# Performance work log

Measured on AMD Instinct MI355X. Metric: run time of the kernel, lower is better.

Reference implementation:

```python
import jax, jax.numpy as jnp
import numpy as np

EMBED_DIM = 1024
NUM_HEADS = 16
HEAD_DIM = EMBED_DIM // NUM_HEADS
T, B = 2048, 2


def setup_inputs() -> dict:
    key = jax.random.key(0)
    ks = jax.random.split(key, 12)
    s = 1.0 / np.sqrt(EMBED_DIM)
    x = jax.random.normal(ks[0], (T, B, EMBED_DIM), dtype=jnp.float32)
    time_decay = jax.random.uniform(ks[1], (T, B, 1), dtype=jnp.float32)
    # causal mask: masked_fill where mask == 0
    attn_mask = jnp.tril(jnp.ones((T, T), dtype=jnp.int32))
    Wq = jax.random.uniform(ks[2], (EMBED_DIM, EMBED_DIM), jnp.float32, -s, s)
    bq = jax.random.uniform(ks[3], (EMBED_DIM,), jnp.float32, -s, s)
    Wk = jax.random.uniform(ks[4], (EMBED_DIM, EMBED_DIM), jnp.float32, -s, s)
    bk = jax.random.uniform(ks[5], (EMBED_DIM,), jnp.float32, -s, s)
    Wv = jax.random.uniform(ks[6], (EMBED_DIM, EMBED_DIM), jnp.float32, -s, s)
    bv = jax.random.uniform(ks[7], (EMBED_DIM,), jnp.float32, -s, s)
    Wo = jax.random.uniform(ks[8], (EMBED_DIM, EMBED_DIM), jnp.float32, -s, s)
    bo = jax.random.uniform(ks[9], (EMBED_DIM,), jnp.float32, -s, s)
    return {"x": x, "time_decay": time_decay, "attn_mask": attn_mask,
            "Wq": Wq, "bq": bq, "Wk": Wk, "bk": bk,
            "Wv": Wv, "bv": bv, "Wo": Wo, "bo": bo}


def reference(x, time_decay, attn_mask, Wq, bq, Wk, bk, Wv, bv, Wo, bo):
    t, b, e = x.shape
    h, d = NUM_HEADS, HEAD_DIM
    # linear (torch: y = x @ W.T + b), then split heads -> (B, H, T, D)
    def proj(W, bias):
        y = jnp.einsum('tbe,fe->tbf', x, W) + bias
        return y.reshape(t, b, h, d).transpose(1, 2, 0, 3)
    Q, K, V = proj(Wq, bq), proj(Wk, bk), proj(Wv, bv)
    scores = jnp.einsum('bhqd,bhkd->bhqk', Q, K) / np.sqrt(d).astype(jnp.float32)
    scores = jnp.where(attn_mask == 0, jnp.float32(-1e9), scores)
    attn = jax.nn.softmax(scores, axis=-1)
    out = jnp.einsum('bhqk,bhkd->bhqd', attn, V)      # (B,H,T,D)
    out = out.transpose(2, 0, 1, 3).reshape(t, b, e)   # (T,B,E)
    out = jnp.einsum('tbe,fe->tbf', out, Wo) + bo
    return out * time_decay
```

## Files before the change

### kernel.cpp

```cpp
#include <hip/hip_runtime.h>


typedef unsigned short u16;
typedef unsigned int u32;
typedef __attribute__((ext_vector_type(8))) short bf16x8_t;
typedef __attribute__((ext_vector_type(4))) float fx4_t;

#define T_SEQ 2048
#define BATCH 2
#define EMB   1024
#define NH    16
#define HD    64
#define MROWS (T_SEQ * BATCH)

#define EXP2F(x) __builtin_amdgcn_exp2f(x)

__device__ __forceinline__ float bf2f(u16 u) {
  union { unsigned int i; float f; } v;
  v.i = ((unsigned int)u) << 16;
  return v.f;
}
__device__ __forceinline__ u16 f2bf(float f) {
  union { float f; unsigned int i; } v;
  v.f = f;
  unsigned int x = v.i;
  unsigned int r = (x + 0x7fffu + ((x >> 16) & 1u)) >> 16;
  return (u16)r;
}
__device__ __forceinline__ u32 fbits(float f) {
  union { float f; u32 i; } v; v.f = f; return v.i;
}

__device__ __forceinline__ void glds16(const void* g, void* l) {
  __builtin_amdgcn_global_load_lds(
      (const __attribute__((address_space(1))) unsigned int*)g,
      (__attribute__((address_space(3))) unsigned int*)l, 16, 0, 0);
}


__global__ void cvt_all(const float* __restrict__ x,
                        const float* __restrict__ wq, const float* __restrict__ wk,
                        const float* __restrict__ wv, const float* __restrict__ wo,
                        u16* __restrict__ xb,
                        u16* __restrict__ wqb, u16* __restrict__ wkb,
                        u16* __restrict__ wvb, u16* __restrict__ wob) {
  int i = blockIdx.x * blockDim.x + threadIdx.x;
  const float* src; u16* dst; int off;
  if (i < 1048576)      { src = x;  dst = xb;  off = i; }
  else if (i < 1310720) { src = wq; dst = wqb; off = i - 1048576; }
  else if (i < 1572864) { src = wk; dst = wkb; off = i - 1310720; }
  else if (i < 1835008) { src = wv; dst = wvb; off = i - 1572864; }
  else                  { src = wo; dst = wob; off = i - 1835008; }
  float4 v = ((const float4*)src)[off];
  ushort4 o;
  o.x = f2bf(v.x); o.y = f2bf(v.y); o.z = f2bf(v.z); o.w = f2bf(v.w);
  ((ushort4*)dst)[off] = o;
}

__global__ __launch_bounds__(256, 3) void gemm_qkv(
    const u16* __restrict__ xb,
    const u16* __restrict__ wq, const u16* __restrict__ wk, const u16* __restrict__ wv,
    const float* __restrict__ bq, const float* __restrict__ bk, const float* __restrict__ bv,
    u16* __restrict__ Qm, u16* __restrict__ Km, u16* __restrict__ VTg) {
  __shared__ short As[2][128 * 64];
  __shared__ short Bs[2][64 * 64];

  const int z = blockIdx.z;
  const u16* W = (z == 0) ? wq : (z == 1) ? wk : wv;
  const float* bias = (z == 0) ? bq : (z == 1) ? bk : bv;

  const int tid = threadIdx.x;
  const int bm = blockIdx.x, bn = blockIdx.y;
  const int lane = tid & 63, w = tid >> 6;
  const int wm = w >> 1, wn = w & 1;
  const int lr = lane & 15, quad = lane >> 4;
  const int r0 = lane >> 3;
  const int c8s = ((lane & 7) ^ r0) * 8;
  const int sw = (lr & 7);

  fx4_t acc[4][2];
#pragma unroll
  for (int i = 0; i < 4; i++)
#pragma unroll
    for (int j = 0; j < 2; j++) acc[i][j] = (fx4_t){0.f, 0.f, 0.f, 0.f};

#define STAGE(kt_, bi_)                                                          \
  {                                                                              \
    const int k0_ = (kt_) * 64;                                                  \
    _Pragma("unroll")                                                            \
    for (int i = 0; i < 4; i++) {             \
      const int rr = w * 32 + i * 8;                                             \
      const int ml = bm * 128 + rr + r0;                                         \
      const int grow = (z == 2) ? (((ml & 2047) << 1) | (ml >> 11)) : ml;        \
      glds16(xb + (size_t)grow * EMB + k0_ + c8s, &As[bi_][rr * 64]);            \
    }                                                                            \
    _Pragma("unroll")                                                            \
    for (int i = 0; i < 2; i++) {              \
      const int rr = w * 16 + i * 8;                                             \
      glds16(W + (size_t)(bn * 64 + rr + r0) * EMB + k0_ + c8s,                  \
             &Bs[bi_][rr * 64]);                                                 \
    }                                                                            \
  }

  const int nkt = EMB / 64;
  STAGE(0, 0);
  __syncthreads();

  for (int kt = 0; kt < nkt; kt++) {
    const int buf = kt & 1;
    if (kt + 1 < nkt) STAGE(kt + 1, buf ^ 1);
#pragma unroll
    for (int ks = 0; ks < 2; ++ks) {
      bf16x8_t a[4], b[2];
#pragma unroll
      for (int i = 0; i < 4; i++)
        a[i] = *(const bf16x8_t*)&As[buf][(wm * 64 + i * 16 + lr) * 64 + (((ks * 4 + quad) ^ sw) * 8)];
#pragma unroll
      for (int j = 0; j < 2; j++)
        b[j] = *(const bf16x8_t*)&Bs[buf][(wn * 32 + j * 16 + lr) * 64 + (((ks * 4 + quad) ^ sw) * 8)];
      if (z == 2) {
#pragma unroll
        for (int i = 0; i < 4; i++)
#pragma unroll
          for (int j = 0; j < 2; j++)
            acc[i][j] = __builtin_amdgcn_mfma_f32_16x16x32_bf16(b[j], a[i], acc[i][j], 0, 0, 0);
      } else {
#pragma unroll
        for (int i = 0; i < 4; i++)
#pragma unroll
          for (int j = 0; j < 2; j++)
            acc[i][j] = __builtin_amdgcn_mfma_f32_16x16x32_bf16(a[i], b[j], acc[i][j], 0, 0, 0);
      }
    }
    __syncthreads();
  }
#undef STAGE

  if (z == 2) {
#pragma unroll
    for (int i = 0; i < 4; i++) {
#pragma unroll
      for (int j = 0; j < 2; j++) {
#pragma unroll
        for (int r = 0; r < 4; r++) {
          const int n = bn * 64 + wn * 32 + j * 16 + quad * 4 + r;
          const int ml = bm * 128 + wm * 64 + i * 16 + lr;
          const int t = ml & 2047, bb = ml >> 11;
          const int h = n >> 6, d = n & 63;
          VTg[((size_t)(bb * NH + h) * HD + d) * T_SEQ + t] = f2bf(acc[i][j][r] + bias[n]);
        }
      }
    }
  } else {
    u16* dst = (z == 0) ? Qm : Km;
#pragma unroll
    for (int i = 0; i < 4; i++) {
#pragma unroll
      for (int j = 0; j < 2; j++) {
        const int n = bn * 64 + wn * 32 + j * 16 + lr;
        const float bsv = bias[n];
#pragma unroll
        for (int r = 0; r < 4; r++) {
          const int m = bm * 128 + wm * 64 + i * 16 + quad * 4 + r;
          dst[(size_t)m * EMB + n] = f2bf(acc[i][j][r] + bsv);
        }
      }
    }
  }
}

__global__ __launch_bounds__(256, 2) void gemm_out(
    const u16* __restrict__ Ob, const u16* __restrict__ wo,
    const float* __restrict__ bo, const float* __restrict__ td,
    float* __restrict__ out) {
  __shared__ short As[64 * 64];
  __shared__ short Bs[128 * 64];

  const int tid = threadIdx.x;
  const int bm = blockIdx.x, bn = blockIdx.y;
  const int lane = tid & 63, w = tid >> 6;
  const int wm = w >> 1, wn = w & 1;
  const int lr = lane & 15, quad = lane >> 4;
  const int r0 = lane >> 3;
  const int c8s = ((lane & 7) ^ r0) * 8;
  const int sw = (lr & 7);

  fx4_t acc[2][4];
#pragma unroll
  for (int i = 0; i < 2; i++)
#pragma unroll
    for (int j = 0; j < 4; j++) acc[i][j] = (fx4_t){0.f, 0.f, 0.f, 0.f};

  for (int k0 = 0; k0 < EMB; k0 += 64) {
#pragma unroll
    for (int i = 0; i < 2; i++) {
      const int rr = w * 16 + i * 8;
      glds16(Ob + (size_t)(bm * 64 + rr + r0) * EMB + k0 + c8s, &As[rr * 64]);
    }
#pragma unroll
    for (int i = 0; i < 4; i++) {
      const int rr = w * 32 + i * 8;
      glds16(wo + (size_t)(bn * 128 + rr + r0) * EMB + k0 + c8s, &Bs[rr * 64]);
    }
    __syncthreads();
#pragma unroll
    for (int ks = 0; ks < 2; ++ks) {
      bf16x8_t a[2], b[4];
#pragma unroll
      for (int i = 0; i < 2; i++)
        a[i] = *(const bf16x8_t*)&As[(wm * 32 + i * 16 + lr) * 64 + (((ks * 4 + quad) ^ sw) * 8)];
#pragma unroll
      for (int j = 0; j < 4; j++)
        b[j] = *(const bf16x8_t*)&Bs[(wn * 64 + j * 16 + lr) * 64 + (((ks * 4 + quad) ^ sw) * 8)];
#pragma unroll
      for (int i = 0; i < 2; i++)
#pragma unroll
        for (int j = 0; j < 4; j++)
          acc[i][j] = __builtin_amdgcn_mfma_f32_16x16x32_bf16(a[i], b[j], acc[i][j], 0, 0, 0);
    }
    __syncthreads();
  }

#pragma unroll
  for (int i = 0; i < 2; i++) {
#pragma unroll
    for (int j = 0; j < 4; j++) {
      const int n = bn * 128 + wn * 64 + j * 16 + lr;
      const float bsv = bo[n];
#pragma unroll
      for (int r = 0; r < 4; r++) {
        const int m = bm * 64 + wm * 32 + i * 16 + quad * 4 + r;
        out[(size_t)m * EMB + n] = (acc[i][j][r] + bsv) * td[m];
      }
    }
  }
}

__global__ __launch_bounds__(256, 2) void attn_bal(
    const u16* __restrict__ Qm, const u16* __restrict__ Km, const u16* __restrict__ VTg,
    u16* __restrict__ Ob) {
  __shared__ short Kd[3][64 * 64];
  __shared__ short Vd[3][64 * 64];
  __shared__ short Ps[4][16 * 72];

  const int blk = blockIdx.x;
  const int bh = blk & 31;
  const int p = blk >> 5;
  const int b = bh >> 4, h = bh & 15;

  const int tid = threadIdx.x;
  const int w = tid >> 6, lane = tid & 63;
  const int lr = lane & 15, quad = lane >> 4;
  const int r0 = lane >> 3;
  const int c8s = ((lane & 7) ^ r0) * 8;
  const int sw = (lr & 7);

  const u16* Qbase = Qm + (size_t)b * EMB + (size_t)h * HD;
  const u16* Kbase = Km + (size_t)b * EMB + (size_t)h * HD;
  const u16* VTb = VTg + (size_t)bh * HD * T_SEQ;

  const float QSCALE = 0.18033688f;

#define STAGE(kt_, buf_)                                                            \
  {                                                                                 \
    const int k0_ = (kt_) * 64;                                                     \
    _Pragma("unroll")                                                               \
    for (int i = 0; i < 2; i++) {                                                   \
      const int rr = w * 16 + i * 8;                                                \
      glds16(Kbase + (size_t)(k0_ + rr + r0) * 2 * EMB + c8s, &Kd[buf_][rr * 64]);  \
      glds16(VTb + (size_t)(rr + r0) * T_SEQ + k0_ + c8s, &Vd[buf_][rr * 64]);      \
    }                                                                               \
  }
#define WAIT4()  asm volatile("s_waitcnt vmcnt(4)" ::: "memory")
#define WAIT0()  asm volatile("s_waitcnt vmcnt(0)" ::: "memory")
#define BAR()    asm volatile("s_barrier" ::: "memory")

  for (int job = 0; job < 2; ++job) {
    const int qt = job ? (31 - p) : p;
    const int qb = qt * 64;

    bf16x8_t qf[2];
#pragma unroll
    for (int ks = 0; ks < 2; ks++) {
      bf16x8_t v = *(const bf16x8_t*)(Qbase + (size_t)(qb + w * 16 + lr) * 2 * EMB + ks * 32 + quad * 8);
      bf16x8_t o;
#pragma unroll
      for (int e = 0; e < 8; e++) o[e] = (short)f2bf(bf2f((u16)v[e]) * QSCALE);
      qf[ks] = o;
    }

    fx4_t acc_o[4];
#pragma unroll
    for (int dn = 0; dn < 4; dn++) acc_o[dn] = (fx4_t){0.f, 0.f, 0.f, 0.f};
    float l_par = 0.f;

    const int nkt = qt + 1;
    STAGE(0, 0);
    if (nkt > 1) { STAGE(1, 1); WAIT4(); } else { WAIT0(); }
    BAR();

    for (int kt = 0; kt < nkt; kt++) {
      const int buf = kt % 3;
      if (kt + 2 < nkt) STAGE(kt + 2, (kt + 2) % 3);

      fx4_t st[4];
#pragma unroll
      for (int nt = 0; nt < 4; nt++) st[nt] = (fx4_t){0.f, 0.f, 0.f, 0.f};
#pragma unroll
      for (int ks = 0; ks < 2; ks++) {
#pragma unroll
        for (int nt = 0; nt < 4; nt++) {
          bf16x8_t kf = *(const bf16x8_t*)&Kd[buf][(nt * 16 + lr) * 64 + (((ks * 4 + quad) ^ sw) * 8)];
          st[nt] = __builtin_amdgcn_mfma_f32_16x16x32_bf16(kf, qf[ks], st[nt], 0, 0, 0);
        }
      }

      bf16x8_t vf[2][4];
#pragma unroll
      for (int ks = 0; ks < 2; ks++)
#pragma unroll
        for (int dn = 0; dn < 4; dn++)
          vf[ks][dn] = *(const bf16x8_t*)&Vd[buf][(dn * 16 + lr) * 64 + (((ks * 4 + quad) ^ sw) * 8)];

      if (kt == qt) {
#pragma unroll
        for (int nt = 0; nt < 4; nt++)
#pragma unroll
          for (int r = 0; r < 4; r++)
            if (nt * 16 + quad * 4 + r > w * 16 + lr) st[nt][r] = -1e30f;
      }

      short* Pw = Ps[w];
#pragma unroll
      for (int nt = 0; nt < 4; nt++) {
        float e0 = EXP2F(st[nt][0]);
        float e1 = EXP2F(st[nt][1]);
        float e2 = EXP2F(st[nt][2]);
        float e3 = EXP2F(st[nt][3]);
        u32 p01 = (fbits(e0) >> 16) | (fbits(e1) & 0xFFFF0000u);
        u32 p23 = (fbits(e2) >> 16) | (fbits(e3) & 0xFFFF0000u);
        uint2 pv; pv.x = p01; pv.y = p23;
        *(uint2*)&Pw[lr * 72 + nt * 16 + quad * 4] = pv;
        l_par += (e0 + e1) + (e2 + e3);
      }

#pragma unroll
      for (int ks = 0; ks < 2; ks++) {
        bf16x8_t pf = *(const bf16x8_t*)&Pw[lr * 72 + ks * 32 + quad * 8];
#pragma unroll
        for (int dn = 0; dn < 4; dn++)
          acc_o[dn] = __builtin_amdgcn_mfma_f32_16x16x32_bf16(pf, vf[ks][dn], acc_o[dn], 0, 0, 0);
      }

      if (kt + 2 < nkt)      { WAIT4(); BAR(); }
      else if (kt + 1 < nkt) { WAIT0(); BAR(); }
    }

    l_par += __shfl_xor(l_par, 16);
    l_par += __shfl_xor(l_par, 32);
    const float inv = 1.0f / l_par;
#pragma unroll
    for (int r = 0; r < 4; r++) {
      const float inv_r = __shfl(inv, quad * 4 + r);
      const int t = qb + w * 16 + quad * 4 + r;
#pragma unroll
      for (int dn = 0; dn < 4; dn++) {
        const int d = dn * 16 + lr;
        Ob[(size_t)(t * BATCH + b) * EMB + h * HD + d] = f2bf(acc_o[dn][r] * inv_r);
      }
    }

    __syncthreads();
  }
#undef STAGE
#undef WAIT4
#undef WAIT0
#undef BAR
}

extern "C" void kernel_launch(void* const* d_in, const int* in_sizes, int n_in,
                              void* d_out, int out_size, void* d_ws, size_t ws_size,
                              hipStream_t stream) {
  const float* x  = (const float*)d_in[0];
  const float* td = (const float*)d_in[1];
  const float* Wq = (const float*)d_in[3];
  const float* bq = (const float*)d_in[4];
  const float* Wk = (const float*)d_in[5];
  const float* bk = (const float*)d_in[6];
  const float* Wv = (const float*)d_in[7];
  const float* bv = (const float*)d_in[8];
  const float* Wo = (const float*)d_in[9];
  const float* bo = (const float*)d_in[10];
  float* out = (float*)d_out;

  char* ws = (char*)d_ws;
  u16* xb  = (u16*)(ws + 0);
  u16* wqb = (u16*)(ws + ((size_t)8  << 20));
  u16* wkb = (u16*)(ws + ((size_t)10 << 20));
  u16* wvb = (u16*)(ws + ((size_t)12 << 20));
  u16* wob = (u16*)(ws + ((size_t)14 << 20));
  u16* Qm  = (u16*)(ws + ((size_t)16 << 20));
  u16* Km  = (u16*)(ws + ((size_t)24 << 20));
  u16* VTg = (u16*)(ws + ((size_t)32 << 20));
  u16* Ob  = xb;

  cvt_all<<<8192, 256, 0, stream>>>(x, Wq, Wk, Wv, Wo, xb, wqb, wkb, wvb, wob);

  gemm_qkv<<<dim3(MROWS / 128, EMB / 64, 3), 256, 0, stream>>>(
      xb, wqb, wkb, wvb, bq, bk, bv, Qm, Km, VTg);

  attn_bal<<<512, 256, 0, stream>>>(Qm, Km, VTg, Ob);

  gemm_out<<<dim3(MROWS / 64, EMB / 128), 256, 0, stream>>>(Ob, wob, bo, td, out);
}
```

Baseline: 190.2 us.

## Double-buffer output projection GEMM and transpose its tile shape

The output projection GEMM now uses two shared-memory stages, so the global-to-LDS load of the next K tile overlaps MFMA work on the current one. This removes one barrier per iteration. The block tile changes from 64x128 to 128x64 (M x N), the grid is adjusted to match, and launch bounds now ask for 3 blocks per CU. The trade-off is twice the LDS per block and a different reuse pattern between the Ob and Wo operands.

```diff
diff --git a/kernel.cpp b/kernel.cpp
--- a/kernel.cpp
+++ b/kernel.cpp
@@ -169,12 +169,12 @@
   }
 }
 
-__global__ __launch_bounds__(256, 2) void gemm_out(
+__global__ __launch_bounds__(256, 3) void gemm_out(
     const u16* __restrict__ Ob, const u16* __restrict__ wo,
     const float* __restrict__ bo, const float* __restrict__ td,
     float* __restrict__ out) {
-  __shared__ short As[64 * 64];
-  __shared__ short Bs[128 * 64];
+  __shared__ short As[2][128 * 64];
+  __shared__ short Bs[2][64 * 64];
 
   const int tid = threadIdx.x;
   const int bm = blockIdx.x, bn = blockIdx.y;
@@ -185,51 +185,64 @@
   const int c8s = ((lane & 7) ^ r0) * 8;
   const int sw = (lr & 7);
 
-  fx4_t acc[2][4];
-#pragma unroll
-  for (int i = 0; i < 2; i++)
-#pragma unroll
-    for (int j = 0; j < 4; j++) acc[i][j] = (fx4_t){0.f, 0.f, 0.f, 0.f};
-
-  for (int k0 = 0; k0 < EMB; k0 += 64) {
-#pragma unroll
-    for (int i = 0; i < 2; i++) {
-      const int rr = w * 16 + i * 8;
-      glds16(Ob + (size_t)(bm * 64 + rr + r0) * EMB + k0 + c8s, &As[rr * 64]);
-    }
-#pragma unroll
-    for (int i = 0; i < 4; i++) {
-      const int rr = w * 32 + i * 8;
-      glds16(wo + (size_t)(bn * 128 + rr + r0) * EMB + k0 + c8s, &Bs[rr * 64]);
+  fx4_t acc[4][2];
+#pragma unroll
+  for (int i = 0; i < 4; i++)
+#pragma unroll
+    for (int j = 0; j < 2; j++) acc[i][j] = (fx4_t){0.f, 0.f, 0.f, 0.f};
+
+#define STAGE(kt_, bi_)                                                          \
+  {                                                                              \
+    const int k0_ = (kt_) * 64;                                                  \
+    _Pragma("unroll")                                                            \
+    for (int i = 0; i < 4; i++) {             \
+      const int rr = w * 32 + i * 8;                                             \
+      glds16(Ob + (size_t)(bm * 128 + rr + r0) * EMB + k0_ + c8s,                \
+             &As[bi_][rr * 64]);                                                 \
+    }                                                                            \
+    _Pragma("unroll")                                                            \
+    for (int i = 0; i < 2; i++) {              \
+      const int rr = w * 16 + i * 8;                                             \
+      glds16(wo + (size_t)(bn * 64 + rr + r0) * EMB + k0_ + c8s,                 \
+             &Bs[bi_][rr * 64]);                                                 \
+    }                                                                            \
+  }
+
+  const int nkt = EMB / 64;
+  STAGE(0, 0);
+  __syncthreads();
+
+  for (int kt = 0; kt < nkt; kt++) {
+    const int buf = kt & 1;
+    if (kt + 1 < nkt) STAGE(kt + 1, buf ^ 1);
+#pragma unroll
+    for (int ks = 0; ks < 2; ++ks) {
+      bf16x8_t a[4], b[2];
+#pragma unroll
+      for (int i = 0; i < 4; i++)
+        a[i] = *(const bf16x8_t*)&As[buf][(wm * 64 + i * 16 + lr) * 64 + (((ks * 4 + quad) ^ sw) * 8)];
+#pragma unroll
+      for (int j = 0; j < 2; j++)
+        b[j] = *(const bf16x8_t*)&Bs[buf][(wn * 32 + j * 16 + lr) * 64 + (((ks * 4 + quad) ^ sw) * 8)];
+#pragma unroll
+      for (int i = 0; i < 4; i++)
+#pragma unroll
+        for (int j = 0; j < 2; j++)
+          acc[i][j] = __builtin_amdgcn_mfma_f32_16x16x32_bf16(a[i], b[j], acc[i][j], 0, 0, 0);
     }
     __syncthreads();
-#pragma unroll
-    for (int ks = 0; ks < 2; ++ks) {
-      bf16x8_t a[2], b[4];
-#pragma unroll
-      for (int i = 0; i < 2; i++)
-        a[i] = *(const bf16x8_t*)&As[(wm * 32 + i * 16 + lr) * 64 + (((ks * 4 + quad) ^ sw) * 8)];
-#pragma unroll
-      for (int j = 0; j < 4; j++)
-        b[j] = *(const bf16x8_t*)&Bs[(wn * 64 + j * 16 + lr) * 64 + (((ks * 4 + quad) ^ sw) * 8)];
-#pragma unroll
-      for (int i = 0; i < 2; i++)
-#pragma unroll
-        for (int j = 0; j < 4; j++)
-          acc[i][j] = __builtin_amdgcn_mfma_f32_16x16x32_bf16(a[i], b[j], acc[i][j], 0, 0, 0);
-    }
-    __syncthreads();
-  }
-
-#pragma unroll
-  for (int i = 0; i < 2; i++) {
-#pragma unroll
-    for (int j = 0; j < 4; j++) {
-      const int n = bn * 128 + wn * 64 + j * 16 + lr;
+  }
+#undef STAGE
+
+#pragma unroll
+  for (int i = 0; i < 4; i++) {
+#pragma unroll
+    for (int j = 0; j < 2; j++) {
+      const int n = bn * 64 + wn * 32 + j * 16 + lr;
       const float bsv = bo[n];
 #pragma unroll
       for (int r = 0; r < 4; r++) {
-        const int m = bm * 64 + wm * 32 + i * 16 + quad * 4 + r;
+        const int m = bm * 128 + wm * 64 + i * 16 + quad * 4 + r;
         out[(size_t)m * EMB + n] = (acc[i][j][r] + bsv) * td[m];
       }
     }
@@ -411,5 +424,5 @@
 
   attn_bal<<<512, 256, 0, stream>>>(Qm, Km, VTg, Ob);
 
-  gemm_out<<<dim3(MROWS / 64, EMB / 128), 256, 0, stream>>>(Ob, wob, bo, td, out);
-}
+  gemm_out<<<dim3(MROWS / 128, EMB / 64), 256, 0, stream>>>(Ob, wob, bo, td, out);
+}
```

Measured after the change: 192.1 us (median of 2 runs). Within noise of the previous version (+1.0%).
